# Optimization experiments

Measured on AMD Instinct MI355X. Metric: run time of the kernel, lower is better.

Reference implementation:

```python
import jax, jax.numpy as jnp
import numpy as np

N_LEVELS = 16
F_PER_LEVEL = 2
LOG2_T = 19
TABLE_SIZE = 1 << LOG2_T
BASE_RES = 16
MAX_RES = 4096
GEO_FEAT = 15
N_PTS = 524288

_b = np.exp((np.log(MAX_RES) - np.log(BASE_RES)) / (N_LEVELS - 1))
RES = np.floor(BASE_RES * _b ** np.arange(N_LEVELS)).astype(np.float32)  # [L]
PRIMES = np.array([1, 2654435761, 805459861], dtype=np.uint32)
# 8 trilinear corner offsets
OFFS = np.array([[(i >> 2) & 1, (i >> 1) & 1, i & 1] for i in range(8)], dtype=np.int32)


def hash_encode(x, table):
    # x: [N,3] in [0,1], table: [L,T,F]
    pos = x[None, :, :] * jnp.asarray(RES)[:, None, None]          # [L,N,3]
    p0 = jnp.floor(pos)
    frac = pos - p0                                                 # [L,N,3]
    corners = p0.astype(jnp.uint32)[:, :, None, :] + jnp.asarray(OFFS.astype(np.uint32))  # [L,N,8,3]
    hp = corners * jnp.asarray(PRIMES)                              # uint32 mul (wraps)
    h = (hp[..., 0] ^ hp[..., 1] ^ hp[..., 2]) & jnp.uint32(TABLE_SIZE - 1)  # [L,N,8]
    w = jnp.where(jnp.asarray(OFFS, bool), frac[:, :, None, :], 1.0 - frac[:, :, None, :]).prod(-1)  # [L,N,8]
    feats = jax.vmap(lambda t, i: t[i])(table, h)                   # [L,N,8,F] hashed gather
    out = (w[..., None] * feats).sum(axis=2)                        # [L,N,F]
    return out.transpose(1, 0, 2).reshape(x.shape[0], N_LEVELS * F_PER_LEVEL)  # [N,32]


def setup_inputs() -> dict:
    key = jax.random.key(0)
    ks = jax.random.split(key, 9)
    positions = jax.random.uniform(ks[0], (N_PTS, 3), dtype=jnp.float32)
    aabb = jnp.array([-1.0, -1.0, -1.0, 1.0, 1.0, 1.0], dtype=jnp.float32)
    table = jax.random.uniform(ks[1], (N_LEVELS, TABLE_SIZE, F_PER_LEVEL), minval=-1e-4, maxval=1e-4, dtype=jnp.float32)
    def lin(k, fan_in, fan_out):
        bound = 1.0 / np.sqrt(fan_in)
        kw, kb = jax.random.split(k)
        return (jax.random.uniform(kw, (fan_in, fan_out), minval=-bound, maxval=bound, dtype=jnp.float32),
                jax.random.uniform(kb, (fan_out,), minval=-bound, maxval=bound, dtype=jnp.float32))
    w1, b1 = lin(ks[2], 32, 64)
    w2, b2 = lin(ks[3], 64, 1 + GEO_FEAT)
    hw1, hb1 = lin(ks[4], GEO_FEAT, 64)
    hw2, hb2 = lin(ks[5], 64, 64)
    hw3, hb3 = lin(ks[6], 64, 3)
    return {"positions": positions, "aabb": aabb, "table": table,
            "w1": w1, "b1": b1, "w2": w2, "b2": b2,
            "hw1": hw1, "hb1": hb1, "hw2": hw2, "hb2": hb2, "hw3": hw3, "hb3": hb3}


def reference(positions, aabb, table, w1, b1, w2, b2, hw1, hb1, hw2, hb2, hw3, hb3):
    aabb_min, aabb_max = aabb[:3], aabb[3:]
    x = (positions - aabb_min) / (aabb_max - aabb_min)              # -> [0,1]
    selector = ((x > 0.0) & (x < 1.0)).all(axis=-1)                 # [N]
    enc = hash_encode(x, table)                                     # [N,32]
    h = jax.nn.relu(enc @ w1 + b1)                                  # [N,64]
    base = h @ w2 + b2                                              # [N,16]
    density_before = base[:, :1]
    embedding = base[:, 1:]
    density = jnp.exp(density_before - 1.0) * selector[:, None].astype(base.dtype)  # trunc_exp(x-1)
    hh = jax.nn.relu(embedding @ hw1 + hb1)
    hh = jax.nn.relu(hh @ hw2 + hb2)
    rgb = jax.nn.sigmoid(hh @ hw3 + hb3)                            # [N,3]
    return rgb, density
```

## Files before the change

kernel.cpp:

```cpp
#include <hip/hip_runtime.h>
#include <math.h>

#define NLV 16
#define TBLBITS 19
#define TBLMASK ((1u << TBLBITS) - 1u)
#define P2 2654435761u
#define P3 805459861u

typedef __attribute__((ext_vector_type(8))) short bf16x8;
typedef __attribute__((ext_vector_type(4))) float f32x4;

__device__ __forceinline__ unsigned f2bf(float f) {
    unsigned u = __builtin_bit_cast(unsigned, f);
    return (u + 0x7fffu + ((u >> 16) & 1u)) >> 16;
}

__global__ __launch_bounds__(256)
void enc_kernel(const float* __restrict__ positions,
                const float* __restrict__ aabb,
                const float* __restrict__ table,
                unsigned* __restrict__ encOut, int npts,
                float r0_, float r1_, float r2_, float r3_,
                float r4_, float r5_, float r6_, float r7_,
                float r8_, float r9_, float r10_, float r11_,
                float r12_, float r13_, float r14_, float r15_)
{
    const unsigned l = blockIdx.y;
    const unsigned p = blockIdx.x * 256u + threadIdx.x;

    const bool s0 = (l & 1u), s1 = (l & 2u), s2 = (l & 4u), s3 = (l & 8u);
    float a0 = s0 ? r1_  : r0_;
    float a1 = s0 ? r3_  : r2_;
    float a2 = s0 ? r5_  : r4_;
    float a3 = s0 ? r7_  : r6_;
    float a4 = s0 ? r9_  : r8_;
    float a5 = s0 ? r11_ : r10_;
    float a6 = s0 ? r13_ : r12_;
    float a7 = s0 ? r15_ : r14_;
    float c0 = s1 ? a1 : a0;
    float c1 = s1 ? a3 : a2;
    float c2 = s1 ? a5 : a4;
    float c3 = s1 ? a7 : a6;
    float d0 = s2 ? c1 : c0;
    float d1 = s2 ? c3 : c2;
    const float r = s3 ? d1 : d0;

    const float px = positions[p * 3 + 0];
    const float py = positions[p * 3 + 1];
    const float pz = positions[p * 3 + 2];
    const float mnx = aabb[0], mny = aabb[1], mnz = aabb[2];
    const float mxx = aabb[3], mxy = aabb[4], mxz = aabb[5];
    const float x0 = (px - mnx) / (mxx - mnx);
    const float x1 = (py - mny) / (mxy - mny);
    const float x2 = (pz - mnz) / (mxz - mnz);

    const float fx = x0 * r, fy = x1 * r, fz = x2 * r;
    const float gx = floorf(fx), gy = floorf(fy), gz = floorf(fz);
    const unsigned cx = (unsigned)gx, cy = (unsigned)gy, cz = (unsigned)gz;
    const float rx = fx - gx, ry = fy - gy, rz = fz - gz;

    const float* tl = table + ((size_t)l << 20);
    float e0 = 0.f, e1 = 0.f;
    const bool xeven = (cx & 1u) == 0u;

    #pragma unroll
    for (int yz = 0; yz < 4; ++yz) {
        const unsigned dy = (yz >> 1) & 1, dz = yz & 1;
        const unsigned base = ((cy + dy) * P2) ^ ((cz + dz) * P3);
        const float wy = dy ? ry : 1.f - ry;
        const float wz = dz ? rz : 1.f - rz;
        const float wyz = wy * wz;
        const float wa = wyz * (1.f - rx);
        const float wb = wyz * rx;
        const unsigned i0 = (cx ^ base) & TBLMASK;

        float f0x, f0y, f1x, f1y;
        if (xeven) {
            const float4 q = *reinterpret_cast<const float4*>(
                tl + ((size_t)(i0 & ~1u) << 1));
            const bool lo = (i0 & 1u) == 0u;
            f0x = lo ? q.x : q.z;  f0y = lo ? q.y : q.w;
            f1x = lo ? q.z : q.x;  f1y = lo ? q.w : q.y;
        } else {
            const unsigned i1 = ((cx + 1u) ^ base) & TBLMASK;
            const float2 qa = *reinterpret_cast<const float2*>(tl + ((size_t)i0 << 1));
            const float2 qb = *reinterpret_cast<const float2*>(tl + ((size_t)i1 << 1));
            f0x = qa.x; f0y = qa.y; f1x = qb.x; f1y = qb.y;
        }
        e0 = fmaf(wa, f0x, e0); e0 = fmaf(wb, f1x, e0);
        e1 = fmaf(wa, f0y, e1); e1 = fmaf(wb, f1y, e1);
    }
    encOut[(size_t)l * npts + p] = f2bf(e0) | (f2bf(e1) << 16);
}

__global__ __launch_bounds__(256)
void prep_weights(const float* __restrict__ w1, const float* __restrict__ w2,
                  const float* __restrict__ hw1, const float* __restrict__ hw2,
                  const float* __restrict__ hw3, unsigned short* __restrict__ wt)
{
    const int i = blockIdx.x * 256 + threadIdx.x;
    if (i >= 12032) return;
    float v = 0.f;
    if (i < 2560) {
        int n = i / 40, k = i % 40;
        if (k < 32) v = w1[k * 64 + n];
    } else if (i < 5120) {
        int j = i - 2560, n = j / 40, k = j % 40;
        if (k < 15) v = hw1[k * 64 + n];
    } else if (i < 6272) {
        int j = i - 5120, n = j / 72, k = j % 72;
        if (k < 64) v = w2[k * 16 + n];
    } else if (i < 10880) {
        int j = i - 6272, n = j / 72, k = j % 72;
        if (k < 64) v = hw2[k * 64 + n];
    } else {
        int j = i - 10880, n = j / 72, k = j % 72;
        if (k < 64 && n < 3) v = hw3[k * 3 + n];
    }
    wt[i] = (unsigned short)f2bf(v);
}

__global__ __launch_bounds__(256)
void mlp_kernel(const unsigned* __restrict__ enc,
                const unsigned short* __restrict__ wt,
                const float* __restrict__ positions,
                const float* __restrict__ aabb,
                const float* __restrict__ b1, const float* __restrict__ b2,
                const float* __restrict__ hb1, const float* __restrict__ hb2,
                const float* __restrict__ hb3,
                float* __restrict__ out, int npts)
{
    __shared__ __align__(16) unsigned short H[4][32 * 72];
    __shared__ float sel_lds[128];

    const int tid  = threadIdx.x;
    const int wave = tid >> 6;
    const int lane = tid & 63;
    const int col  = lane & 15;
    const int lgrp = lane >> 4;
    const int blockPt = blockIdx.x * 128;
    const int wavePt  = blockPt + wave * 32;

    if (lane < 32) {
        const int gp = wavePt + lane;
        const float px = positions[gp * 3 + 0];
        const float py = positions[gp * 3 + 1];
        const float pz = positions[gp * 3 + 2];
        const float mnx = aabb[0], mny = aabb[1], mnz = aabb[2];
        const float mxx = aabb[3], mxy = aabb[4], mxz = aabb[5];
        const float x0 = (px - mnx) / (mxx - mnx);
        const float x1 = (py - mny) / (mxy - mny);
        const float x2 = (pz - mnz) / (mxz - mnz);
        const bool sel = (x0 > 0.f) && (x0 < 1.f) && (x1 > 0.f) && (x1 < 1.f) &&
                         (x2 > 0.f) && (x2 < 1.f);
        sel_lds[wave * 32 + lane] = sel ? 1.f : 0.f;
    }

    float bias1[4], biasH1[4], biasH2[4];
    #pragma unroll
    for (int nt = 0; nt < 4; ++nt) {
        bias1[nt]  = b1[nt * 16 + col];
        biasH1[nt] = hb1[nt * 16 + col];
        biasH2[nt] = hb2[nt * 16 + col];
    }
    const float bias2 = b2[col];
    const float biasH3 = (col < 3) ? hb3[col] : 0.f;

    bf16x8 a1[2];
    #pragma unroll
    for (int mt = 0; mt < 2; ++mt) {
        const int ptl = wavePt + mt * 16 + col;
        uint4 v;
        v.x = enc[(size_t)(lgrp * 4 + 0) * npts + ptl];
        v.y = enc[(size_t)(lgrp * 4 + 1) * npts + ptl];
        v.z = enc[(size_t)(lgrp * 4 + 2) * npts + ptl];
        v.w = enc[(size_t)(lgrp * 4 + 3) * npts + ptl];
        a1[mt] = __builtin_bit_cast(bf16x8, v);
    }

    const unsigned short* w1t = wt;
    const unsigned short* w3t = wt + 2560;
    const unsigned short* w2t = wt + 5120;
    const unsigned short* w4t = wt + 6272;
    const unsigned short* w5t = wt + 10880;
    unsigned short* Hw = H[wave];

    {
        f32x4 acc[2][4];
        #pragma unroll
        for (int mt = 0; mt < 2; ++mt)
            #pragma unroll
            for (int nt = 0; nt < 4; ++nt) {
                const float b = bias1[nt];
                acc[mt][nt] = (f32x4){b, b, b, b};
            }
        #pragma unroll
        for (int nt = 0; nt < 4; ++nt) {
            const bf16x8 b = *reinterpret_cast<const bf16x8*>(
                w1t + (nt * 16 + col) * 40 + lgrp * 8);
            #pragma unroll
            for (int mt = 0; mt < 2; ++mt)
                acc[mt][nt] = __builtin_amdgcn_mfma_f32_16x16x32_bf16(
                    a1[mt], b, acc[mt][nt], 0, 0, 0);
        }
        #pragma unroll
        for (int mt = 0; mt < 2; ++mt)
            #pragma unroll
            for (int nt = 0; nt < 4; ++nt)
                #pragma unroll
                for (int rr = 0; rr < 4; ++rr) {
                    const float h = fmaxf(acc[mt][nt][rr], 0.f);
                    const int row = mt * 16 + lgrp * 4 + rr;
                    Hw[row * 72 + nt * 16 + col] = (unsigned short)f2bf(h);
                }
    }

    {
        f32x4 acc[2];
        #pragma unroll
        for (int mt = 0; mt < 2; ++mt)
            acc[mt] = (f32x4){bias2, bias2, bias2, bias2};
        #pragma unroll
        for (int ks = 0; ks < 2; ++ks) {
            const bf16x8 b = *reinterpret_cast<const bf16x8*>(
                w2t + col * 72 + ks * 32 + lgrp * 8);
            #pragma unroll
            for (int mt = 0; mt < 2; ++mt) {
                const bf16x8 a = *reinterpret_cast<const bf16x8*>(
                    Hw + (mt * 16 + col) * 72 + ks * 32 + lgrp * 8);
                acc[mt] = __builtin_amdgcn_mfma_f32_16x16x32_bf16(
                    a, b, acc[mt], 0, 0, 0);
            }
        }
        #pragma unroll
        for (int mt = 0; mt < 2; ++mt)
            #pragma unroll
            for (int rr = 0; rr < 4; ++rr) {
                const float base = acc[mt][rr];
                const int row = mt * 16 + lgrp * 4 + rr;
                if (col == 0) {
                    const float dn = __expf(base - 1.f) * sel_lds[wave * 32 + row];
                    out[(size_t)npts * 3 + wavePt + row] = dn;
                } else {
                    Hw[row * 72 + (col - 1)] = (unsigned short)f2bf(base);
                }
            }
        if (lane < 32) {
            const int row = lane;
            Hw[row * 72 + 15] = 0;
            const uint4 z4 = {0, 0, 0, 0};
            *reinterpret_cast<uint4*>(Hw + row * 72 + 16) = z4;
            *reinterpret_cast<uint4*>(Hw + row * 72 + 24) = z4;
        }
    }

    {
        f32x4 acc[2][4];
        #pragma unroll
        for (int mt = 0; mt < 2; ++mt)
            #pragma unroll
            for (int nt = 0; nt < 4; ++nt) {
                const float b = biasH1[nt];
                acc[mt][nt] = (f32x4){b, b, b, b};
            }
        bf16x8 a[2];
        #pragma unroll
        for (int mt = 0; mt < 2; ++mt)
            a[mt] = *reinterpret_cast<const bf16x8*>(
                Hw + (mt * 16 + col) * 72 + lgrp * 8);
        #pragma unroll
        for (int nt = 0; nt < 4; ++nt) {
            const bf16x8 b = *reinterpret_cast<const bf16x8*>(
                w3t + (nt * 16 + col) * 40 + lgrp * 8);
            #pragma unroll
            for (int mt = 0; mt < 2; ++mt)
                acc[mt][nt] = __builtin_amdgcn_mfma_f32_16x16x32_bf16(
                    a[mt], b, acc[mt][nt], 0, 0, 0);
        }
        #pragma unroll
        for (int mt = 0; mt < 2; ++mt)
            #pragma unroll
            for (int nt = 0; nt < 4; ++nt)
                #pragma unroll
                for (int rr = 0; rr < 4; ++rr) {
                    const float h = fmaxf(acc[mt][nt][rr], 0.f);
                    const int row = mt * 16 + lgrp * 4 + rr;
                    Hw[row * 72 + nt * 16 + col] = (unsigned short)f2bf(h);
                }
    }

    {
        f32x4 acc[2][4];
        #pragma unroll
        for (int mt = 0; mt < 2; ++mt)
            #pragma unroll
            for (int nt = 0; nt < 4; ++nt) {
                const float b = biasH2[nt];
                acc[mt][nt] = (f32x4){b, b, b, b};
            }
        #pragma unroll
        for (int ks = 0; ks < 2; ++ks) {
            bf16x8 a[2];
            #pragma unroll
            for (int mt = 0; mt < 2; ++mt)
                a[mt] = *reinterpret_cast<const bf16x8*>(
                    Hw + (mt * 16 + col) * 72 + ks * 32 + lgrp * 8);
            #pragma unroll
            for (int nt = 0; nt < 4; ++nt) {
                const bf16x8 b = *reinterpret_cast<const bf16x8*>(
                    w4t + (nt * 16 + col) * 72 + ks * 32 + lgrp * 8);
                #pragma unroll
                for (int mt = 0; mt < 2; ++mt)
                    acc[mt][nt] = __builtin_amdgcn_mfma_f32_16x16x32_bf16(
                        a[mt], b, acc[mt][nt], 0, 0, 0);
            }
        }
        #pragma unroll
        for (int mt = 0; mt < 2; ++mt)
            #pragma unroll
            for (int nt = 0; nt < 4; ++nt)
                #pragma unroll
                for (int rr = 0; rr < 4; ++rr) {
                    const float h = fmaxf(acc[mt][nt][rr], 0.f);
                    const int row = mt * 16 + lgrp * 4 + rr;
                    Hw[row * 72 + nt * 16 + col] = (unsigned short)f2bf(h);
                }
    }

    {
        f32x4 acc[2];
        #pragma unroll
        for (int mt = 0; mt < 2; ++mt)
            acc[mt] = (f32x4){biasH3, biasH3, biasH3, biasH3};
        #pragma unroll
        for (int ks = 0; ks < 2; ++ks) {
            const bf16x8 b = *reinterpret_cast<const bf16x8*>(
                w5t + col * 72 + ks * 32 + lgrp * 8);
            #pragma unroll
            for (int mt = 0; mt < 2; ++mt) {
                const bf16x8 a = *reinterpret_cast<const bf16x8*>(
                    Hw + (mt * 16 + col) * 72 + ks * 32 + lgrp * 8);
                acc[mt] = __builtin_amdgcn_mfma_f32_16x16x32_bf16(
                    a, b, acc[mt], 0, 0, 0);
            }
        }
        if (col < 3) {
            #pragma unroll
            for (int mt = 0; mt < 2; ++mt)
                #pragma unroll
                for (int rr = 0; rr < 4; ++rr) {
                    const float v = acc[mt][rr];
                    const float rgb = 1.f / (1.f + __expf(-v));
                    const int row = mt * 16 + lgrp * 4 + rr;
                    out[(size_t)(wavePt + row) * 3 + col] = rgb;
                }
        }
    }
}

extern "C" void kernel_launch(void* const* d_in, const int* in_sizes, int n_in,
                              void* d_out, int out_size, void* d_ws, size_t ws_size,
                              hipStream_t stream) {
    const float* positions = (const float*)d_in[0];
    const float* aabb      = (const float*)d_in[1];
    const float* table     = (const float*)d_in[2];
    const float* w1  = (const float*)d_in[3];
    const float* b1  = (const float*)d_in[4];
    const float* w2  = (const float*)d_in[5];
    const float* b2  = (const float*)d_in[6];
    const float* hw1 = (const float*)d_in[7];
    const float* hb1 = (const float*)d_in[8];
    const float* hw2 = (const float*)d_in[9];
    const float* hb2 = (const float*)d_in[10];
    const float* hw3 = (const float*)d_in[11];
    const float* hb3 = (const float*)d_in[12];
    float* out = (float*)d_out;

    const int npts = in_sizes[0] / 3;

    unsigned* encbuf = (unsigned*)d_ws;
    unsigned short* wt =
        (unsigned short*)((char*)d_ws + (size_t)npts * 16 * 4);

    float R[NLV];
    const double bb = exp((log(4096.0) - log(16.0)) / 15.0);
    for (int l = 0; l < NLV; ++l)
        R[l] = (float)floor(16.0 * pow(bb, (double)l));

    prep_weights<<<47, 256, 0, stream>>>(w1, w2, hw1, hw2, hw3, wt);

    dim3 egrid(npts / 256, NLV);
    enc_kernel<<<egrid, 256, 0, stream>>>(
        positions, aabb, table, encbuf, npts,
        R[0], R[1], R[2], R[3], R[4], R[5], R[6], R[7],
        R[8], R[9], R[10], R[11], R[12], R[13], R[14], R[15]);

    mlp_kernel<<<npts / 128, 256, 0, stream>>>(
        encbuf, wt, positions, aabb, b1, b2, hb1, hb2, hb3, out, npts);
}
```

Measured before the change: 320.7 us.

## Repack coarse hash levels into dense grids and gather them inside MLP kernel

The four coarsest levels (res 16/23/33/48) have no more cells than the hash table holds, so a small pre-pass writes each level's hashed features into a dense x-major 3D array. The MLP kernel then interpolates those levels itself from the compact dense layout, with better locality and paired z-neighbour loads, and moves them across lanes with ds_bpermute. The encoding kernel now runs only the 12 finer levels, which cuts encoding-buffer writes and reads by a quarter. The cost is an extra small kernel, more register pressure and a serial gather latency at the head of the MLP kernel, plus one lane group computing while others wait.

```diff
diff --git a/kernel.cpp b/kernel.cpp
--- a/kernel.cpp
+++ b/kernel.cpp
@@ -7,12 +7,40 @@
 #define P2 2654435761u
 #define P3 805459861u
 
+#define D_BASE0 0
+#define D_BASE1 4914
+#define D_BASE2 18738
+#define D_BASE3 58044
+#define D_TOTAL 175694
+
 typedef __attribute__((ext_vector_type(8))) short bf16x8;
 typedef __attribute__((ext_vector_type(4))) float f32x4;
 
 __device__ __forceinline__ unsigned f2bf(float f) {
     unsigned u = __builtin_bit_cast(unsigned, f);
     return (u + 0x7fffu + ((u >> 16) & 1u)) >> 16;
+}
+
+__global__ __launch_bounds__(256)
+void dense_repack(const float* __restrict__ table, float* __restrict__ dense)
+{
+    const int i = blockIdx.x * 256 + threadIdx.x;
+    if (i >= D_TOTAL) return;
+    int g, lo, dim;
+    if (i < 4913)                       { g = 0; lo = i;           dim = 17; }
+    else if (i >= D_BASE1 && i < 18738) { g = 1; lo = i - D_BASE1; dim = 24; }
+    else if (i >= D_BASE2 && i < 58042) { g = 2; lo = i - D_BASE2; dim = 34; }
+    else if (i >= D_BASE3 && i < 175693){ g = 3; lo = i - D_BASE3; dim = 49; }
+    else return;
+    const unsigned z = (unsigned)lo % (unsigned)dim;
+    const unsigned t = (unsigned)lo / (unsigned)dim;
+    const unsigned y = t % (unsigned)dim;
+    const unsigned x = t / (unsigned)dim;
+    const unsigned h = (x ^ y * P2 ^ z * P3) & TBLMASK;
+    const float* tl = table + ((size_t)g << 20);
+    const float2 v = *reinterpret_cast<const float2*>(tl + ((size_t)h << 1));
+    dense[(size_t)i * 2 + 0] = v.x;
+    dense[(size_t)i * 2 + 1] = v.y;
 }
 
 __global__ __launch_bounds__(256)
@@ -25,7 +53,7 @@
                 float r8_, float r9_, float r10_, float r11_,
                 float r12_, float r13_, float r14_, float r15_)
 {
-    const unsigned l = blockIdx.y;
+    const unsigned l = blockIdx.y + 4u;
     const unsigned p = blockIdx.x * 256u + threadIdx.x;
 
     const bool s0 = (l & 1u), s1 = (l & 2u), s2 = (l & 4u), s3 = (l & 8u);
@@ -90,7 +118,7 @@
         e0 = fmaf(wa, f0x, e0); e0 = fmaf(wb, f1x, e0);
         e1 = fmaf(wa, f0y, e1); e1 = fmaf(wb, f1y, e1);
     }
-    encOut[(size_t)l * npts + p] = f2bf(e0) | (f2bf(e1) << 16);
+    encOut[(size_t)(l - 4u) * npts + p] = f2bf(e0) | (f2bf(e1) << 16);
 }
 
 __global__ __launch_bounds__(256)
@@ -120,9 +148,43 @@
     wt[i] = (unsigned short)f2bf(v);
 }
 
+__device__ __forceinline__ unsigned dense_gather(
+    const float* __restrict__ dt, int g, float x0, float x1, float x2)
+{
+    const float r  = (g & 2) ? ((g & 1) ? 48.f : 33.f) : ((g & 1) ? 23.f : 16.f);
+    const int  dim = (g & 2) ? ((g & 1) ? 49 : 34) : ((g & 1) ? 24 : 17);
+    const int  bse = (g & 2) ? ((g & 1) ? D_BASE3 : D_BASE2)
+                             : ((g & 1) ? D_BASE1 : D_BASE0);
+    const float fx = x0 * r, fy = x1 * r, fz = x2 * r;
+    const float gx = floorf(fx), gy = floorf(fy), gz = floorf(fz);
+    const int cx = (int)gx, cy = (int)gy, cz = (int)gz;
+    const float rx = fx - gx, ry = fy - gy, rz = fz - gz;
+    float e0 = 0.f, e1 = 0.f;
+    #pragma unroll
+    for (int xy = 0; xy < 4; ++xy) {
+        const int dx = xy >> 1, dy = xy & 1;
+        const int row = ((cx + dx) * dim + (cy + dy)) * dim + cz + bse;
+        const float wxy = (dx ? rx : 1.f - rx) * (dy ? ry : 1.f - ry);
+        const float wa = wxy * (1.f - rz), wb = wxy * rz;
+        float f0x, f0y, f1x, f1y;
+        if (!(row & 1)) {
+            const float4 q = *reinterpret_cast<const float4*>(dt + ((size_t)row << 1));
+            f0x = q.x; f0y = q.y; f1x = q.z; f1y = q.w;
+        } else {
+            const float2 qa = *reinterpret_cast<const float2*>(dt + ((size_t)row << 1));
+            const float2 qb = *reinterpret_cast<const float2*>(dt + ((size_t)(row + 1) << 1));
+            f0x = qa.x; f0y = qa.y; f1x = qb.x; f1y = qb.y;
+        }
+        e0 = fmaf(wa, f0x, e0); e0 = fmaf(wb, f1x, e0);
+        e1 = fmaf(wa, f0y, e1); e1 = fmaf(wb, f1y, e1);
+    }
+    return f2bf(e0) | (f2bf(e1) << 16);
+}
+
 __global__ __launch_bounds__(256)
 void mlp_kernel(const unsigned* __restrict__ enc,
                 const unsigned short* __restrict__ wt,
+                const float* __restrict__ dense,
                 const float* __restrict__ positions,
                 const float* __restrict__ aabb,
                 const float* __restrict__ b1, const float* __restrict__ b2,
@@ -141,13 +203,14 @@
     const int blockPt = blockIdx.x * 128;
     const int wavePt  = blockPt + wave * 32;
 
+    const float mnx = aabb[0], mny = aabb[1], mnz = aabb[2];
+    const float mxx = aabb[3], mxy = aabb[4], mxz = aabb[5];
+
     if (lane < 32) {
         const int gp = wavePt + lane;
         const float px = positions[gp * 3 + 0];
         const float py = positions[gp * 3 + 1];
         const float pz = positions[gp * 3 + 2];
-        const float mnx = aabb[0], mny = aabb[1], mnz = aabb[2];
-        const float mxx = aabb[3], mxy = aabb[4], mxz = aabb[5];
         const float x0 = (px - mnx) / (mxx - mnx);
         const float x1 = (py - mny) / (mxy - mny);
         const float x2 = (pz - mnz) / (mxz - mnz);
@@ -170,11 +233,28 @@
     #pragma unroll
     for (int mt = 0; mt < 2; ++mt) {
         const int ptl = wavePt + mt * 16 + col;
+        const float px = positions[ptl * 3 + 0];
+        const float py = positions[ptl * 3 + 1];
+        const float pz = positions[ptl * 3 + 2];
+        const float x0 = (px - mnx) / (mxx - mnx);
+        const float x1 = (py - mny) / (mxy - mny);
+        const float x2 = (pz - mnz) / (mxz - mnz);
+        const unsigned dv = dense_gather(dense, lgrp, x0, x1, x2);
+        const int er = (lgrp == 0) ? 0 : (lgrp * 4 - 4);
+        const unsigned e0v = enc[(size_t)(er + 0) * npts + ptl];
+        const unsigned e1v = enc[(size_t)(er + 1) * npts + ptl];
+        const unsigned e2v = enc[(size_t)(er + 2) * npts + ptl];
+        const unsigned e3v = enc[(size_t)(er + 3) * npts + ptl];
+        const int cbase = col * 4;
+        const unsigned d0 = (unsigned)__builtin_amdgcn_ds_bpermute(cbase,       (int)dv);
+        const unsigned d1 = (unsigned)__builtin_amdgcn_ds_bpermute(cbase + 64,  (int)dv);
+        const unsigned d2 = (unsigned)__builtin_amdgcn_ds_bpermute(cbase + 128, (int)dv);
+        const unsigned d3 = (unsigned)__builtin_amdgcn_ds_bpermute(cbase + 192, (int)dv);
         uint4 v;
-        v.x = enc[(size_t)(lgrp * 4 + 0) * npts + ptl];
-        v.y = enc[(size_t)(lgrp * 4 + 1) * npts + ptl];
-        v.z = enc[(size_t)(lgrp * 4 + 2) * npts + ptl];
-        v.w = enc[(size_t)(lgrp * 4 + 3) * npts + ptl];
+        v.x = (lgrp == 0) ? d0 : e0v;
+        v.y = (lgrp == 0) ? d1 : e1v;
+        v.z = (lgrp == 0) ? d2 : e2v;
+        v.w = (lgrp == 0) ? d3 : e3v;
         a1[mt] = __builtin_bit_cast(bf16x8, v);
     }
 
@@ -379,8 +459,8 @@
     const int npts = in_sizes[0] / 3;
 
     unsigned* encbuf = (unsigned*)d_ws;
-    unsigned short* wt =
-        (unsigned short*)((char*)d_ws + (size_t)npts * 16 * 4);
+    unsigned short* wt = (unsigned short*)((char*)d_ws + (size_t)npts * 12 * 4);
+    float* dense = (float*)((char*)d_ws + (size_t)npts * 12 * 4 + 24064);
 
     float R[NLV];
     const double bb = exp((log(4096.0) - log(16.0)) / 15.0);
@@ -388,13 +468,14 @@
         R[l] = (float)floor(16.0 * pow(bb, (double)l));
 
     prep_weights<<<47, 256, 0, stream>>>(w1, w2, hw1, hw2, hw3, wt);
-
-    dim3 egrid(npts / 256, NLV);
+    dense_repack<<<(D_TOTAL + 255) / 256, 256, 0, stream>>>(table, dense);
+
+    dim3 egrid(npts / 256, 12);
     enc_kernel<<<egrid, 256, 0, stream>>>(
         positions, aabb, table, encbuf, npts,
         R[0], R[1], R[2], R[3], R[4], R[5], R[6], R[7],
         R[8], R[9], R[10], R[11], R[12], R[13], R[14], R[15]);
 
     mlp_kernel<<<npts / 128, 256, 0, stream>>>(
-        encbuf, wt, positions, aabb, b1, b2, hb1, hb2, hb3, out, npts);
-}
+        encbuf, wt, dense, positions, aabb, b1, b2, hb1, hb2, hb3, out, npts);
+}
```

Result: slower. 327.4 us (+2.1%).
